# Kernel tuning notes

Hardware: AMD Instinct MI355X
Metric: run time of the kernel (lower is better)

Reference implementation:

```python
import jax, jax.numpy as jnp
import numpy as np

MUL = 64          # multiplicity of 0e and 1o channels
N_NODES = 50000
N_EDGES = 800000
NUM_NEIGHBORS = 16.0
SILU_NORM = 1.679177  # e3nn normalize2mom constant for silu


def setup_inputs() -> dict:
    key = jax.random.key(0)
    ks = jax.random.split(key, 9)
    node_in = jax.random.normal(ks[0], (N_NODES, 4 * MUL), dtype=jnp.float32)  # 64x0e + 64x1o
    edge_src = jax.random.randint(ks[1], (N_EDGES,), 0, N_NODES)
    edge_dst = jax.random.randint(ks[2], (N_EDGES,), 0, N_NODES)
    edge_attr = jax.random.normal(ks[3], (N_EDGES, 4), dtype=jnp.float32)      # 1x0e + 1x1o
    edge_len_emb = jax.random.uniform(ks[4], (N_EDGES, 10), dtype=jnp.float32)
    # tensor-product path weights [mul_in, mul_out] (mul_edge = 1)
    w_00_0 = jax.random.normal(ks[5], (MUL, MUL), dtype=jnp.float32)  # 0e x 0e -> 0e
    w_11_0 = jax.random.normal(ks[6], (MUL, MUL), dtype=jnp.float32)  # 1o x 1o -> 0e
    w_01_1 = jax.random.normal(ks[7], (MUL, MUL), dtype=jnp.float32)  # 0e x 1o -> 1o
    w_10_1 = jax.random.normal(ks[8], (MUL, MUL), dtype=jnp.float32)  # 1o x 0e -> 1o
    kf = jax.random.split(jax.random.fold_in(key, 1), 2)
    fc_w1 = jax.random.normal(kf[0], (10, 64), dtype=jnp.float32)
    fc_w2 = jax.random.normal(kf[1], (64, 1), dtype=jnp.float32)
    return {"node_in": node_in, "edge_attr": edge_attr, "edge_len_emb": edge_len_emb,
            "w_00_0": w_00_0, "w_11_0": w_11_0, "w_01_1": w_01_1, "w_10_1": w_10_1,
            "fc_w1": fc_w1, "fc_w2": fc_w2, "edge_src": edge_src, "edge_dst": edge_dst}


def reference(node_in, edge_attr, edge_len_emb, w_00_0, w_11_0, w_01_1, w_10_1,
              fc_w1, fc_w2, edge_src, edge_dst):
    # gather source node features per edge
    src = node_in[edge_src]                      # [E, 256]
    s0 = src[:, :MUL]                            # [E, mul]       scalars 0e
    s1 = src[:, MUL:].reshape(-1, MUL, 3)        # [E, mul, 3]    vectors 1o
    a0 = edge_attr[:, 0:1]                       # [E, 1]   edge 0e
    a1 = edge_attr[:, 1:4]                       # [E, 3]   edge 1o

    # fully-connected tensor product: path norm 1/sqrt(num_paths * fan_in)
    alpha = np.float32(1.0 / np.sqrt(2.0 * MUL))
    inv_sqrt3 = np.float32(1.0 / np.sqrt(3.0))
    # scalar output: 0e x 0e -> 0e  and  1o . 1o -> 0e (CG = delta/sqrt(3))
    out0 = alpha * (jnp.einsum('ei,io->eo', s0 * a0, w_00_0)
                    + inv_sqrt3 * jnp.einsum('eim,em,io->eo', s1, a1, w_11_0))   # [E, mul]
    # vector output: 0e x 1o -> 1o  and  1o x 0e -> 1o (CG = identity)
    out1 = alpha * (jnp.einsum('ei,io,em->eom', s0, w_01_1, a1)
                    + jnp.einsum('eim,io->eom', s1 * a0[:, :, None], w_10_1))     # [E, mul, 3]
    msg_ang = jnp.concatenate([out0, out1.reshape(-1, 3 * MUL)], axis=1)         # [E, 256]

    # radial MLP gate: FullyConnectedNet([10, 64, 1], silu)
    h = jax.nn.silu(edge_len_emb @ fc_w1 / np.float32(np.sqrt(10.0))) * np.float32(SILU_NORM)
    msg_rad = h @ fc_w2 / np.float32(np.sqrt(64.0))                              # [E, 1]

    messages = msg_ang * msg_rad
    agg = jax.ops.segment_sum(messages, edge_dst, num_segments=node_in.shape[0])
    return agg / np.float32(np.sqrt(NUM_NEIGHBORS))
```

## Files before the change

kernel.cpp:

```cpp
#include <hip/hip_runtime.h>

#define NE 800000
#define NN 50000
#define MAXD 64
#define FILL_BLK (NE / 256)
#define XC_BLK (NN / 8)
#define PSTR 516

typedef __attribute__((ext_vector_type(4))) unsigned short ushort4v;
typedef __attribute__((ext_vector_type(4))) _Float16 f16x4;
typedef __attribute__((ext_vector_type(4))) float f32x4;

static constexpr float ALPHA      = 0.08838834764831845f;
static constexpr float INV3       = 0.57735026918962576f;
static constexpr float INV_SQRT10 = 0.31622776601683794f;
static constexpr float SILU_NORM  = 1.679177f;
static constexpr float QSCALE     = ALPHA * 0.25f;

__device__ __forceinline__ unsigned short f2h_bits(float f) {
  _Float16 h = (_Float16)f;
  unsigned short b;
  __builtin_memcpy(&b, &h, 2);
  return b;
}
__device__ __forceinline__ float h2f_bits(unsigned int b) {
  unsigned short s = (unsigned short)b;
  _Float16 h;
  __builtin_memcpy(&h, &s, 2);
  return (float)h;
}
__device__ __forceinline__ unsigned int packh2(float lo, float hi) {
  return (unsigned int)f2h_bits(lo) | ((unsigned int)f2h_bits(hi) << 16);
}

__global__ __launch_bounds__(256) void k_combo(
    const float* __restrict__ X, unsigned short* __restrict__ Xp,
    const float* __restrict__ attr, const float* __restrict__ emb,
    const float* __restrict__ w1, const float* __restrict__ w2,
    const int* __restrict__ esrc, const int* __restrict__ edst,
    int* __restrict__ cur, uint4* __restrict__ ell) {
  __shared__ float lds[2816];
  if (blockIdx.x < FILL_BLK) {
    int eb = blockIdx.x * 256;
    int e = eb + threadIdx.x;
    int dst = edst[e];
    int src = esrc[e];
    float4 a = *(const float4*)(attr + (size_t)e * 4);
    int slot = atomicAdd(&cur[dst], 1);

    const float* ebase = emb + (size_t)eb * 10;
#pragma unroll
    for (int j = 0; j < 10; j++)
      lds[j * 256 + threadIdx.x] = ebase[j * 256 + threadIdx.x];
    __syncthreads();
    const float* x = lds + threadIdx.x * 10;
    float r = 0.f;
#pragma unroll
    for (int j = 0; j < 64; j++) {
      float d = 0.f;
#pragma unroll
      for (int k = 0; k < 10; k++) d = fmaf(x[k], w1[k * 64 + j], d);
      d *= INV_SQRT10;
      float h = d * __builtin_amdgcn_rcpf(1.f + __expf(-d)) * SILU_NORM;
      r = fmaf(h, w2[j], r);
    }
    r *= 0.125f * QSCALE;
    if (slot < MAXD) {
      ell[dst * MAXD + slot] =
          make_uint4((unsigned)src, packh2(r * a.x, r * a.y),
                     packh2(r * a.z, r * a.w), 0u);
    }
  } else {
    int n0 = (blockIdx.x - FILL_BLK) * 8;
    const float4* Xs = (const float4*)(X + (size_t)n0 * 256);
    float4* L4 = (float4*)lds;
    L4[threadIdx.x] = Xs[threadIdx.x];
    L4[256 + threadIdx.x] = Xs[256 + threadIdx.x];
    __syncthreads();
    int o = threadIdx.x & 63;
    int nl = threadIdx.x >> 6;
#pragma unroll
    for (int ii = 0; ii < 2; ii++) {
      int n_l = nl + ii * 4;
      const float* row = lds + n_l * 256;
      ushort4v v;
      v[0] = f2h_bits(row[o]);
      v[1] = f2h_bits(row[64 + 3 * o]);
      v[2] = f2h_bits(row[64 + 3 * o + 1]);
      v[3] = f2h_bits(row[64 + 3 * o + 2]);
      *(ushort4v*)(Xp + (size_t)(n0 + n_l) * 256 + o * 4) = v;
    }
  }
}

__device__ __forceinline__ void eop(unsigned int q01, unsigned int q23,
                                    ushort4v y, float& u0, float& u1,
                                    float& v0, float& v1, float& v2, float& w0,
                                    float& w1, float& w2) {
  float q0 = h2f_bits(q01), q1 = h2f_bits(q01 >> 16);
  float q2 = h2f_bits(q23), q3 = h2f_bits(q23 >> 16);
  float x0 = h2f_bits(y[0]), xa = h2f_bits(y[1]);
  float xb = h2f_bits(y[2]), xc = h2f_bits(y[3]);
  u0 = fmaf(q0, x0, u0);
  u1 = fmaf(q1, xa, u1);
  u1 = fmaf(q2, xb, u1);
  u1 = fmaf(q3, xc, u1);
  v0 = fmaf(q1, x0, v0);
  v1 = fmaf(q2, x0, v1);
  v2 = fmaf(q3, x0, v2);
  w0 = fmaf(q0, xa, w0);
  w1 = fmaf(q0, xb, w1);
  w2 = fmaf(q0, xc, w2);
}

__global__ __launch_bounds__(1024, 1) void k_aggpost(
    const int* __restrict__ cur, const uint4* __restrict__ ell,
    const unsigned short* __restrict__ Xp, const float* __restrict__ W00,
    const float* __restrict__ W11, const float* __restrict__ W01,
    const float* __restrict__ W10, float* __restrict__ out) {
  __shared__ unsigned short Pl[16 * PSTR];
  int w = threadIdx.x >> 6;
  int o = threadIdx.x & 63;
  int nb = blockIdx.x * 16;
  int n = nb + w;

  int d = cur[n];
  if (d > MAXD) d = MAXD;
  const uint4* base = ell + n * MAXD;

  float u0 = 0.f, u1 = 0.f, v0 = 0.f, v1 = 0.f, v2 = 0.f;
  float w0 = 0.f, w1 = 0.f, w2 = 0.f;
  int i = 0;
  for (; i + 4 <= d; i += 4) {
    uint4 rec[4];
    ushort4v y[4];
#pragma unroll
    for (int q = 0; q < 4; q++) rec[q] = base[i + q];
#pragma unroll
    for (int q = 0; q < 4; q++)
      y[q] = *(const ushort4v*)(Xp + ((size_t)rec[q].x << 8) + (o << 2));
#pragma unroll
    for (int q = 0; q < 4; q++)
      eop(rec[q].y, rec[q].z, y[q], u0, u1, v0, v1, v2, w0, w1, w2);
  }
  for (; i < d; i++) {
    uint4 rec = base[i];
    ushort4v y = *(const ushort4v*)(Xp + ((size_t)rec.x << 8) + (o << 2));
    eop(rec.y, rec.z, y, u0, u1, v0, v1, v2, w0, w1, w2);
  }

  int rb = w * PSTR;
  Pl[rb + 0 * 64 + o] = f2h_bits(u0);
  Pl[rb + 1 * 64 + o] = f2h_bits(u1 * INV3);
  Pl[rb + 2 * 64 + o] = f2h_bits(v0);
  Pl[rb + 3 * 64 + o] = f2h_bits(v1);
  Pl[rb + 4 * 64 + o] = f2h_bits(v2);
  Pl[rb + 5 * 64 + o] = f2h_bits(w0);
  Pl[rb + 6 * 64 + o] = f2h_bits(w1);
  Pl[rb + 7 * 64 + o] = f2h_bits(w2);
  __syncthreads();

  int j = w & 3;
  int part = w >> 2;
  int lr = o & 15, lq = o >> 4;
  int col = 16 * j + lr;

  int c0 = (part == 0) ? 0 : 2 + (part - 1);
  int c1 = (part == 0) ? 1 : 5 + (part - 1);
  const float* Wp0 = (part == 0) ? W00 : W01;
  const float* Wp1 = (part == 0) ? W11 : W10;

  f16x4 a0[4], a1[4], b0[4], b1[4];
#pragma unroll
  for (int kq = 0; kq < 4; kq++) {
    int od = kq * 16 + lq * 4;
    ushort4v t0 = *(const ushort4v*)(Pl + lr * PSTR + c0 * 64 + od);
    ushort4v t1 = *(const ushort4v*)(Pl + lr * PSTR + c1 * 64 + od);
    __builtin_memcpy(&a0[kq], &t0, 8);
    __builtin_memcpy(&a1[kq], &t1, 8);
#pragma unroll
    for (int ii = 0; ii < 4; ii++) {
      int row = od + ii;
      b0[kq][ii] = (_Float16)Wp0[row * 64 + col];
      b1[kq][ii] = (_Float16)Wp1[row * 64 + col];
    }
  }

  f32x4 acc = {0.f, 0.f, 0.f, 0.f};
#pragma unroll
  for (int kq = 0; kq < 4; kq++) {
    acc = __builtin_amdgcn_mfma_f32_16x16x16f16(a0[kq], b0[kq], acc, 0, 0, 0);
    acc = __builtin_amdgcn_mfma_f32_16x16x16f16(a1[kq], b1[kq], acc, 0, 0, 0);
  }

  if (part == 0) {
#pragma unroll
    for (int r = 0; r < 4; r++)
      out[(size_t)(nb + lq * 4 + r) * 256 + col] = acc[r];
  } else {
    int m = part - 1;
#pragma unroll
    for (int r = 0; r < 4; r++)
      out[(size_t)(nb + lq * 4 + r) * 256 + 64 + 3 * col + m] = acc[r];
  }
}

extern "C" void kernel_launch(void* const* d_in, const int* in_sizes, int n_in,
                              void* d_out, int out_size, void* d_ws,
                              size_t ws_size, hipStream_t stream) {
  const float* node_in = (const float*)d_in[0];
  const float* edge_attr = (const float*)d_in[1];
  const float* emb = (const float*)d_in[2];
  const float* w00 = (const float*)d_in[3];
  const float* w11 = (const float*)d_in[4];
  const float* w01 = (const float*)d_in[5];
  const float* w10 = (const float*)d_in[6];
  const float* fw1 = (const float*)d_in[7];
  const float* fw2 = (const float*)d_in[8];
  const int* esrc = (const int*)d_in[9];
  const int* edst = (const int*)d_in[10];
  float* out = (float*)d_out;

  char* ws = (char*)d_ws;
  unsigned short* Xp = (unsigned short*)ws; ws += (size_t)NN * 256 * 2;
  uint4* ell = (uint4*)ws;                  ws += (size_t)NN * MAXD * 16;
  int* cur = (int*)ws;                      ws += (size_t)NN * 4;

  (void)hipMemsetAsync(cur, 0, (size_t)NN * 4, stream);
  k_combo<<<FILL_BLK + XC_BLK, 256, 0, stream>>>(
      node_in, Xp, edge_attr, emb, fw1, fw2, esrc, edst, cur, ell);
  k_aggpost<<<NN / 16, 1024, 0, stream>>>(cur, ell, Xp, w00, w11, w01, w10,
                                          out);
}
```

Measured before the change: 145.9 us.

## Split wavefront halves across edges with 16-byte gathers in aggregation

The aggregation kernel now has each half of a wavefront process alternate edges. Each lane loads 8 fp16 values (two output channels) per gather instead of 4, and the partial sums are combined with a cross-half shuffle before writing to shared memory. This halves the serial loop trip count and widens each memory access, at the cost of doubling accumulator registers and padding odd-degree nodes with zero-weight records. The launch bound is raised to allow two blocks per CU, and index math is widened to size_t.

```diff
diff --git a/kernel.cpp b/kernel.cpp
--- a/kernel.cpp
+++ b/kernel.cpp
@@ -8,6 +8,7 @@
 #define PSTR 516
 
 typedef __attribute__((ext_vector_type(4))) unsigned short ushort4v;
+typedef __attribute__((ext_vector_type(8))) unsigned short ushort8;
 typedef __attribute__((ext_vector_type(4))) _Float16 f16x4;
 typedef __attribute__((ext_vector_type(4))) float f32x4;
 
@@ -66,7 +67,7 @@
     }
     r *= 0.125f * QSCALE;
     if (slot < MAXD) {
-      ell[dst * MAXD + slot] =
+      ell[(size_t)dst * MAXD + slot] =
           make_uint4((unsigned)src, packh2(r * a.x, r * a.y),
                      packh2(r * a.z, r * a.w), 0u);
     }
@@ -93,76 +94,131 @@
   }
 }
 
-__device__ __forceinline__ void eop(unsigned int q01, unsigned int q23,
-                                    ushort4v y, float& u0, float& u1,
-                                    float& v0, float& v1, float& v2, float& w0,
-                                    float& w1, float& w2) {
+__device__ __forceinline__ void eop2(unsigned int q01, unsigned int q23,
+                                     ushort8 y, float& u0a, float& u1a,
+                                     float& v0a, float& v1a, float& v2a,
+                                     float& w0a, float& w1a, float& w2a,
+                                     float& u0b, float& u1b, float& v0b,
+                                     float& v1b, float& v2b, float& w0b,
+                                     float& w1b, float& w2b) {
   float q0 = h2f_bits(q01), q1 = h2f_bits(q01 >> 16);
   float q2 = h2f_bits(q23), q3 = h2f_bits(q23 >> 16);
   float x0 = h2f_bits(y[0]), xa = h2f_bits(y[1]);
   float xb = h2f_bits(y[2]), xc = h2f_bits(y[3]);
-  u0 = fmaf(q0, x0, u0);
-  u1 = fmaf(q1, xa, u1);
-  u1 = fmaf(q2, xb, u1);
-  u1 = fmaf(q3, xc, u1);
-  v0 = fmaf(q1, x0, v0);
-  v1 = fmaf(q2, x0, v1);
-  v2 = fmaf(q3, x0, v2);
-  w0 = fmaf(q0, xa, w0);
-  w1 = fmaf(q0, xb, w1);
-  w2 = fmaf(q0, xc, w2);
-}
-
-__global__ __launch_bounds__(1024, 1) void k_aggpost(
+  u0a = fmaf(q0, x0, u0a);
+  u1a = fmaf(q1, xa, u1a);
+  u1a = fmaf(q2, xb, u1a);
+  u1a = fmaf(q3, xc, u1a);
+  v0a = fmaf(q1, x0, v0a);
+  v1a = fmaf(q2, x0, v1a);
+  v2a = fmaf(q3, x0, v2a);
+  w0a = fmaf(q0, xa, w0a);
+  w1a = fmaf(q0, xb, w1a);
+  w2a = fmaf(q0, xc, w2a);
+  float z0 = h2f_bits(y[4]), za = h2f_bits(y[5]);
+  float zb = h2f_bits(y[6]), zc = h2f_bits(y[7]);
+  u0b = fmaf(q0, z0, u0b);
+  u1b = fmaf(q1, za, u1b);
+  u1b = fmaf(q2, zb, u1b);
+  u1b = fmaf(q3, zc, u1b);
+  v0b = fmaf(q1, z0, v0b);
+  v1b = fmaf(q2, z0, v1b);
+  v2b = fmaf(q3, z0, v2b);
+  w0b = fmaf(q0, za, w0b);
+  w1b = fmaf(q0, zb, w1b);
+  w2b = fmaf(q0, zc, w2b);
+}
+
+__global__ __launch_bounds__(1024, 2) void k_aggpost(
     const int* __restrict__ cur, const uint4* __restrict__ ell,
     const unsigned short* __restrict__ Xp, const float* __restrict__ W00,
     const float* __restrict__ W11, const float* __restrict__ W01,
     const float* __restrict__ W10, float* __restrict__ out) {
   __shared__ unsigned short Pl[16 * PSTR];
   int w = threadIdx.x >> 6;
-  int o = threadIdx.x & 63;
+  int l = threadIdx.x & 63;
+  int half = l >> 5;
+  int lp = l & 31;
   int nb = blockIdx.x * 16;
   int n = nb + w;
 
   int d = cur[n];
   if (d > MAXD) d = MAXD;
-  const uint4* base = ell + n * MAXD;
-
-  float u0 = 0.f, u1 = 0.f, v0 = 0.f, v1 = 0.f, v2 = 0.f;
-  float w0 = 0.f, w1 = 0.f, w2 = 0.f;
+  const uint4* base = ell + (size_t)n * MAXD;
+
+  float u0a = 0.f, u1a = 0.f, v0a = 0.f, v1a = 0.f, v2a = 0.f;
+  float w0a = 0.f, w1a = 0.f, w2a = 0.f;
+  float u0b = 0.f, u1b = 0.f, v0b = 0.f, v1b = 0.f, v2b = 0.f;
+  float w0b = 0.f, w1b = 0.f, w2b = 0.f;
+
+  int np = (d + 1) >> 1;
   int i = 0;
-  for (; i + 4 <= d; i += 4) {
+  for (; i + 4 <= np; i += 4) {
     uint4 rec[4];
-    ushort4v y[4];
-#pragma unroll
-    for (int q = 0; q < 4; q++) rec[q] = base[i + q];
+    ushort8 y[4];
+#pragma unroll
+    for (int q = 0; q < 4; q++) {
+      int idx = 2 * (i + q) + half;
+      int cidx = idx < d ? idx : d - 1;
+      rec[q] = base[cidx];
+      if (idx >= d) {
+        rec[q].y = 0u;
+        rec[q].z = 0u;
+      }
+    }
 #pragma unroll
     for (int q = 0; q < 4; q++)
-      y[q] = *(const ushort4v*)(Xp + ((size_t)rec[q].x << 8) + (o << 2));
+      y[q] = *(const ushort8*)(Xp + ((size_t)rec[q].x << 8) + (lp << 3));
 #pragma unroll
     for (int q = 0; q < 4; q++)
-      eop(rec[q].y, rec[q].z, y[q], u0, u1, v0, v1, v2, w0, w1, w2);
-  }
-  for (; i < d; i++) {
-    uint4 rec = base[i];
-    ushort4v y = *(const ushort4v*)(Xp + ((size_t)rec.x << 8) + (o << 2));
-    eop(rec.y, rec.z, y, u0, u1, v0, v1, v2, w0, w1, w2);
-  }
+      eop2(rec[q].y, rec[q].z, y[q], u0a, u1a, v0a, v1a, v2a, w0a, w1a, w2a,
+           u0b, u1b, v0b, v1b, v2b, w0b, w1b, w2b);
+  }
+  for (; i < np; i++) {
+    int idx = 2 * i + half;
+    int cidx = idx < d ? idx : d - 1;
+    uint4 rec = base[cidx];
+    if (idx >= d) {
+      rec.y = 0u;
+      rec.z = 0u;
+    }
+    ushort8 y = *(const ushort8*)(Xp + ((size_t)rec.x << 8) + (lp << 3));
+    eop2(rec.y, rec.z, y, u0a, u1a, v0a, v1a, v2a, w0a, w1a, w2a, u0b, u1b,
+         v0b, v1b, v2b, w0b, w1b, w2b);
+  }
+
+  u0a += __shfl_xor(u0a, 32, 64);
+  u1a += __shfl_xor(u1a, 32, 64);
+  v0a += __shfl_xor(v0a, 32, 64);
+  v1a += __shfl_xor(v1a, 32, 64);
+  v2a += __shfl_xor(v2a, 32, 64);
+  w0a += __shfl_xor(w0a, 32, 64);
+  w1a += __shfl_xor(w1a, 32, 64);
+  w2a += __shfl_xor(w2a, 32, 64);
+  u0b += __shfl_xor(u0b, 32, 64);
+  u1b += __shfl_xor(u1b, 32, 64);
+  v0b += __shfl_xor(v0b, 32, 64);
+  v1b += __shfl_xor(v1b, 32, 64);
+  v2b += __shfl_xor(v2b, 32, 64);
+  w0b += __shfl_xor(w0b, 32, 64);
+  w1b += __shfl_xor(w1b, 32, 64);
+  w2b += __shfl_xor(w2b, 32, 64);
 
   int rb = w * PSTR;
-  Pl[rb + 0 * 64 + o] = f2h_bits(u0);
-  Pl[rb + 1 * 64 + o] = f2h_bits(u1 * INV3);
-  Pl[rb + 2 * 64 + o] = f2h_bits(v0);
-  Pl[rb + 3 * 64 + o] = f2h_bits(v1);
-  Pl[rb + 4 * 64 + o] = f2h_bits(v2);
-  Pl[rb + 5 * 64 + o] = f2h_bits(w0);
-  Pl[rb + 6 * 64 + o] = f2h_bits(w1);
-  Pl[rb + 7 * 64 + o] = f2h_bits(w2);
+  int om = 2 * lp + half;
+  Pl[rb + 0 * 64 + om] = f2h_bits(half ? u0b : u0a);
+  Pl[rb + 1 * 64 + om] = f2h_bits((half ? u1b : u1a) * INV3);
+  Pl[rb + 2 * 64 + om] = f2h_bits(half ? v0b : v0a);
+  Pl[rb + 3 * 64 + om] = f2h_bits(half ? v1b : v1a);
+  Pl[rb + 4 * 64 + om] = f2h_bits(half ? v2b : v2a);
+  Pl[rb + 5 * 64 + om] = f2h_bits(half ? w0b : w0a);
+  Pl[rb + 6 * 64 + om] = f2h_bits(half ? w1b : w1a);
+  Pl[rb + 7 * 64 + om] = f2h_bits(half ? w2b : w2a);
   __syncthreads();
 
   int j = w & 3;
   int part = w >> 2;
-  int lr = o & 15, lq = o >> 4;
+  int lr = l & 15, lq = l >> 4;
   int col = 16 * j + lr;
 
   int c0 = (part == 0) ? 0 : 2 + (part - 1);
```

Result: slower. 156.5 us (+7.2%).
